# Optimization experiments

Measured on AMD Instinct MI355X. Metric: run time of the kernel, lower is better.

The kernel has to match this reference:

```python
import jax, jax.numpy as jnp
import numpy as np

B, T, OBS = 16, 4095, 128
HID, NH, FF, NL = 256, 8, 1024, 4
DH = HID // NH
ACT = 32
KEPS = 0.001   # performer kernel_epsilon (generalized attention default)
LNEPS = 1e-6   # flax LayerNorm default eps


def setup_inputs() -> dict:
    key = jax.random.key(0)
    ks = list(jax.random.split(key, 16))
    s = 0.02
    r = lambda k, shape: jax.random.normal(k, shape, jnp.float32) * s
    return {
        "hidden_state": jnp.zeros((B, 1, HID), jnp.float32),
        "ins": jax.random.normal(ks[0], (B, T, OBS), jnp.float32),
        "resets": jax.random.randint(ks[1], (B,), 0, 2).astype(bool),
        "emb_W": r(ks[2], (OBS, HID)), "emb_b": jnp.zeros((HID,), jnp.float32),
        "Wq": r(ks[3], (NL, HID, NH, DH)), "bq": jnp.zeros((NL, NH, DH), jnp.float32),
        "Wk": r(ks[4], (NL, HID, NH, DH)), "bk": jnp.zeros((NL, NH, DH), jnp.float32),
        "Wv": r(ks[5], (NL, HID, NH, DH)), "bv": jnp.zeros((NL, NH, DH), jnp.float32),
        "Wo": r(ks[6], (NL, NH, DH, HID)), "bo": jnp.zeros((NL, HID), jnp.float32),
        "ln1_s": jnp.ones((NL, HID), jnp.float32), "ln1_b": jnp.zeros((NL, HID), jnp.float32),
        "W1": r(ks[7], (NL, HID, FF)), "b1": jnp.zeros((NL, FF), jnp.float32),
        "W2": r(ks[8], (NL, FF, HID)), "b2": jnp.zeros((NL, HID), jnp.float32),
        "ln2_s": jnp.ones((NL, HID), jnp.float32), "ln2_b": jnp.zeros((NL, HID), jnp.float32),
        "qp_W": r(ks[9], (HID, ACT)), "qp_b": jnp.zeros((ACT,), jnp.float32),
    }


def layer_norm(x, scale, bias):
    m = x.mean(-1, keepdims=True)
    v = ((x - m) ** 2).mean(-1, keepdims=True)
    return (x - m) * jax.lax.rsqrt(v + LNEPS) * scale + bias


def favor_attention(q, k, v):
    # FAVOR+ generalized attention with deterministic relu features (no random
    # projection, make_fast_generalized_attention defaults), bidirectional,
    # renormalized. q,k,v: [B, L, H, Dh]; feature dim M == Dh.
    qp = jax.nn.relu(q) + KEPS
    kp = jax.nn.relu(k) + KEPS
    kv = jnp.einsum('blhm,blhd->bhmd', kp, v)            # [B,H,M,Dh]
    num = jnp.einsum('blhm,bhmd->blhd', qp, kv)           # [B,L,H,Dh]
    den = jnp.einsum('blhm,bhm->blh', qp, kp.sum(axis=1))  # [B,L,H]
    return num / den[..., None]


def encoder_block(x, Wq, bq, Wk, bk, Wv, bv, Wo, bo, ln1_s, ln1_b, W1, b1, W2, b2, ln2_s, ln2_b):
    q = jnp.einsum('bld,dhm->blhm', x, Wq) + bq
    k = jnp.einsum('bld,dhm->blhm', x, Wk) + bk
    v = jnp.einsum('bld,dhm->blhm', x, Wv) + bv
    a = favor_attention(q, k, v)
    o = jnp.einsum('blhm,hmd->bld', a, Wo) + bo
    x = o + o  # faithful to source: x = attn(x); x = x + dropout(x)
    x = layer_norm(x, ln1_s, ln1_b)
    h = jax.nn.relu(x @ W1 + b1) @ W2 + b2
    h = h + h  # same residual quirk on the FFN branch
    return layer_norm(h, ln2_s, ln2_b)


def reference(hidden_state, ins, resets, emb_W, emb_b, Wq, bq, Wk, bk, Wv, bv, Wo, bo, ln1_s, ln1_b, W1, b1, W2, b2, ln2_s, ln2_b, qp_W, qp_b):
    emb = ins @ emb_W + emb_b                         # [B, T, HID]
    hs = jnp.where(resets[:, None, None], 0.0, hidden_state)
    x = jnp.concatenate([hs, emb], axis=-2)           # [B, 1+T, HID]
    for i in range(NL):
        x = encoder_block(x, Wq[i], bq[i], Wk[i], bk[i], Wv[i], bv[i], Wo[i], bo[i],
                          ln1_s[i], ln1_b[i], W1[i], b1[i], W2[i], b2[i], ln2_s[i], ln2_b[i])
    new_hidden = x[..., 0:1, :]                       # carry token
    q_vals = new_hidden @ qp_W + qp_b                 # [B, 1, ACT]
    return new_hidden, q_vals
```

## Files before the change

### kernel.cpp

```cpp
#include <hip/hip_runtime.h>


typedef unsigned short bf16_t;
typedef __attribute__((ext_vector_type(8))) short short8;
typedef __attribute__((ext_vector_type(4))) float float4v;

#define NB 16
#define LSEQ 4096
#define MROWS (NB * LSEQ)
#define HIDD 256
#define NHEAD 8
#define DHEAD 32
#define FFD 1024
#define NLAY 4
#define KEPS_F 1e-3f
#define LNEPS_F 1e-6f
#define KV_ELEMS (NB * NHEAD * 32 * 33)

__device__ __forceinline__ float b2f(bf16_t h) {
    return __uint_as_float(((unsigned int)h) << 16);
}
__device__ __forceinline__ bf16_t f2b(float f) {
    unsigned int u = __float_as_uint(f);
    u += 0x7fffu + ((u >> 16) & 1u);
    return (bf16_t)(u >> 16);
}

#define GLOAD_LDS16(g, l)                                                     \
    __builtin_amdgcn_global_load_lds(                                         \
        (const __attribute__((address_space(1))) void*)(g),                   \
        (__attribute__((address_space(3))) void*)(l), 16, 0, 0)

__global__ __launch_bounds__(256) void conv_transpose_kernel(
    const float* __restrict__ in, bf16_t* __restrict__ out, int R, int C,
    size_t ils, size_t ols)
{
    __shared__ float tile[32][33];
    const size_t ib = (size_t)blockIdx.z * ils;
    const size_t ob = (size_t)blockIdx.z * ols;
    const int r0 = blockIdx.y * 32, c0 = blockIdx.x * 32;
    const int tx = threadIdx.x & 31, ty = threadIdx.x >> 5;
#pragma unroll
    for (int rr = ty; rr < 32; rr += 8)
        tile[rr][tx] = in[ib + (size_t)(r0 + rr) * C + c0 + tx];
    __syncthreads();
#pragma unroll
    for (int rr = ty; rr < 32; rr += 8)
        out[ob + (size_t)(c0 + rr) * R + r0 + tx] = f2b(tile[tx][rr]);
}

__global__ __launch_bounds__(256) void concat_bias_kernel(
    const float* __restrict__ bq, const float* __restrict__ bk,
    const float* __restrict__ bv, float* __restrict__ bqkv)
{
    const int l = blockIdx.x, j = threadIdx.x;
    bqkv[l * 768 + j]       = bq[l * 256 + j];
    bqkv[l * 768 + 256 + j] = bk[l * 256 + j];
    bqkv[l * 768 + 512 + j] = bv[l * 256 + j];
}

__global__ __launch_bounds__(256) void prep_a_kernel(
    const float* __restrict__ ins, bf16_t* __restrict__ Ain)
{
    const int row = blockIdx.x * 2 + (threadIdx.x >> 7);
    const int j = threadIdx.x & 127;
    const int b = row >> 12, l = row & (LSEQ - 1);
    bf16_t v = 0;
    if (l != 0) v = f2b(ins[((size_t)b * 4095 + (l - 1)) * 128 + j]);
    Ain[(size_t)row * 128 + j] = v;
}

__global__ __launch_bounds__(256) void fix_row0_kernel(
    const float* __restrict__ hidden, const int* __restrict__ resets,
    bf16_t* __restrict__ X)
{
    const int b = blockIdx.x, j = threadIdx.x;
    float v = resets[b] ? 0.f : hidden[b * HIDD + j];
    X[((size_t)b * LSEQ) * HIDD + j] = f2b(v);
}

template <int MODE>
__global__ __launch_bounds__(512) void gemm_mfma(
    const bf16_t* __restrict__ A, const bf16_t* __restrict__ WT,
    const float* __restrict__ bias, bf16_t* __restrict__ C,
    int M, int N, int K, int lda, int ldc)
{
    __shared__ __align__(16) bf16_t As[128 * 64];
    __shared__ __align__(16) bf16_t Bs[256 * 64];
    const int tid = threadIdx.x;
    const int wave = tid >> 6, lane = tid & 63;

    const int Nn = N >> 8;
    const int id = blockIdx.x;
    const int s = id >> 3;
    const int bm = ((id & 7) + ((s / Nn) << 3)) * 128;
    const int bn = (s % Nn) * 256;

    const int quad = lane >> 4, mr = lane & 15;
    const int mxor = mr & 7;
    const int wm0 = (wave & 1) * 64;
    const int wn0 = (wave >> 1) * 64;

    float4v acc[4][4];
#pragma unroll
    for (int i = 0; i < 4; i++)
#pragma unroll
        for (int j = 0; j < 4; j++) acc[i][j] = (float4v)(0.f);

    for (int k0 = 0; k0 < K; k0 += 64) {
#pragma unroll
        for (int it = 0; it < 2; it++) {
            const int c = it * 512 + tid;
            const int r = c >> 3;
            const int kofs = ((c & 7) ^ (r & 7)) * 8;
            GLOAD_LDS16(A + (size_t)(bm + r) * lda + k0 + kofs, &As[c * 8]);
        }
#pragma unroll
        for (int it = 0; it < 4; it++) {
            const int c = it * 512 + tid;
            const int r = c >> 3;
            const int kofs = ((c & 7) ^ (r & 7)) * 8;
            GLOAD_LDS16(WT + (size_t)(bn + r) * K + k0 + kofs, &Bs[c * 8]);
        }
        __syncthreads();
#pragma unroll
        for (int kk = 0; kk < 8; kk += 4) {
            short8 a[4], b[4];
#pragma unroll
            for (int i = 0; i < 4; i++)
                a[i] = *(const short8*)&As[((wm0 + i * 16 + mr) * 8 + ((quad + kk) ^ mxor)) * 8];
#pragma unroll
            for (int j = 0; j < 4; j++)
                b[j] = *(const short8*)&Bs[((wn0 + j * 16 + mr) * 8 + ((quad + kk) ^ mxor)) * 8];
#pragma unroll
            for (int i = 0; i < 4; i++)
#pragma unroll
                for (int j = 0; j < 4; j++)
                    acc[i][j] = __builtin_amdgcn_mfma_f32_16x16x32_bf16(
                        a[i], b[j], acc[i][j], 0, 0, 0);
        }
        __syncthreads();
    }

    float bcol[4];
#pragma unroll
    for (int j = 0; j < 4; j++) bcol[j] = bias[bn + wn0 + j * 16 + mr];
#pragma unroll
    for (int i = 0; i < 4; i++) {
#pragma unroll
        for (int r = 0; r < 4; r++) {
            const int grow = bm + wm0 + i * 16 + quad * 4 + r;
            bf16_t* crow = C + (size_t)grow * ldc + bn + wn0 + mr;
#pragma unroll
            for (int j = 0; j < 4; j++) {
                float v = acc[i][j][r] + bcol[j];
                if (MODE == 1) v = fmaxf(v, 0.f);
                crow[j * 16] = f2b(v);
            }
        }
    }
}

__global__ __launch_bounds__(512) void gemm_ln_mfma(
    const bf16_t* __restrict__ A, const bf16_t* __restrict__ WT,
    const float* __restrict__ bias, const float* __restrict__ sc,
    const float* __restrict__ bi, bf16_t* __restrict__ out,
    int K, int lda)
{
    __shared__ __align__(16) bf16_t As[128 * 64];
    __shared__ __align__(16) bf16_t Bs[256 * 64];
    __shared__ float red[8][64][2];
    __shared__ float fin[128][2];

    const int tid = threadIdx.x;
    const int wave = tid >> 6, lane = tid & 63;
    const int bm = blockIdx.x * 128;
    const int quad = lane >> 4, mr = lane & 15;
    const int mxor = mr & 7;
    const int wm0 = (wave & 1) * 64;
    const int wn0 = (wave >> 1) * 64;

    float4v acc[4][4];
#pragma unroll
    for (int i = 0; i < 4; i++)
#pragma unroll
        for (int j = 0; j < 4; j++) acc[i][j] = (float4v)(0.f);

    for (int k0 = 0; k0 < K; k0 += 64) {
#pragma unroll
        for (int it = 0; it < 6; it++) {
            const int c = it * 512 + tid;
            if (c < 1024) {
                const int r = c >> 3;
                const int kofs = ((c & 7) ^ (r & 7)) * 8;
                GLOAD_LDS16(A + (size_t)(bm + r) * lda + k0 + kofs, &As[c * 8]);
            } else {
                const int cb = c - 1024;
                const int r = cb >> 3;
                const int kofs = ((cb & 7) ^ (r & 7)) * 8;
                GLOAD_LDS16(WT + (size_t)r * K + k0 + kofs, &Bs[cb * 8]);
            }
        }
        __syncthreads();
#pragma unroll
        for (int kk = 0; kk < 8; kk += 4) {
            short8 a[4], b[4];
#pragma unroll
            for (int i = 0; i < 4; i++)
                a[i] = *(const short8*)&As[((wm0 + i * 16 + mr) * 8 + ((quad + kk) ^ mxor)) * 8];
#pragma unroll
            for (int j = 0; j < 4; j++)
                b[j] = *(const short8*)&Bs[((wn0 + j * 16 + mr) * 8 + ((quad + kk) ^ mxor)) * 8];
#pragma unroll
            for (int i = 0; i < 4; i++)
#pragma unroll
                for (int j = 0; j < 4; j++)
                    acc[i][j] = __builtin_amdgcn_mfma_f32_16x16x32_bf16(
                        a[i], b[j], acc[i][j], 0, 0, 0);
        }
        __syncthreads();
    }

    float bcol[4];
#pragma unroll
    for (int j = 0; j < 4; j++) bcol[j] = bias[wn0 + j * 16 + mr];

#pragma unroll
    for (int i = 0; i < 4; i++) {
#pragma unroll
        for (int r = 0; r < 4; r++) {
            float s = 0.f, s2 = 0.f;
#pragma unroll
            for (int j = 0; j < 4; j++) {
                const float v = 2.0f * (acc[i][j][r] + bcol[j]);
                s += v; s2 += v * v;
            }
#pragma unroll
            for (int off = 1; off < 16; off <<= 1) {
                s  += __shfl_xor(s, off, 64);
                s2 += __shfl_xor(s2, off, 64);
            }
            if (mr == 0) {
                const int rl = i * 16 + quad * 4 + r;
                red[wave][rl][0] = s;
                red[wave][rl][1] = s2;
            }
        }
    }
    __syncthreads();
    if (tid < 256) {
        const int R = tid >> 1, p = tid & 1;
        const int mh = R >> 6, rl = R & 63;
        fin[R][p] = red[mh][rl][p] + red[mh + 2][rl][p]
                  + red[mh + 4][rl][p] + red[mh + 6][rl][p];
    }
    __syncthreads();

    float scv[4], biv[4];
#pragma unroll
    for (int j = 0; j < 4; j++) {
        scv[j] = sc[wn0 + j * 16 + mr];
        biv[j] = bi[wn0 + j * 16 + mr];
    }
#pragma unroll
    for (int i = 0; i < 4; i++) {
#pragma unroll
        for (int r = 0; r < 4; r++) {
            const int R = wm0 + i * 16 + quad * 4 + r;
            const float mean = fin[R][0] * (1.0f / 256.0f);
            const float var  = fin[R][1] * (1.0f / 256.0f) - mean * mean;
            const float rs = rsqrtf(var + LNEPS_F);
            bf16_t* crow = out + (size_t)(bm + R) * 256 + wn0 + mr;
#pragma unroll
            for (int j = 0; j < 4; j++) {
                const float v = 2.0f * (acc[i][j][r] + bcol[j]);
                crow[j * 16] = f2b((v - mean) * rs * scv[j] + biv[j]);
            }
        }
    }
}

__global__ __launch_bounds__(512) void gemm_favor_ln_mfma(
    const bf16_t* __restrict__ QKV, const float* __restrict__ KV,
    const bf16_t* __restrict__ WT, const float* __restrict__ bias,
    const float* __restrict__ sc, const float* __restrict__ bi,
    bf16_t* __restrict__ out)
{
    __shared__ __align__(16) bf16_t As[128 * 64];
    __shared__ __align__(16) bf16_t Bs[256 * 64];
    __shared__ __align__(16) bf16_t kvT[NHEAD * 34 * 36];
    __shared__ float red[8][64][2];
    __shared__ float fin[128][2];

    const int tid = threadIdx.x;
    const int wave = tid >> 6, lane = tid & 63;
    const int bm = blockIdx.x * 128;
    const int b = bm >> 12;
    const int quad = lane >> 4, mr = lane & 15;
    const int mxor = mr & 7;
    const int wm0 = (wave & 1) * 64;
    const int wn0 = (wave >> 1) * 64;

    for (int e = tid; e < NHEAD * 34 * 32; e += 512) {
        const int h = e / (34 * 32);
        const int rem = e - h * (34 * 32);
        const int d = rem >> 5, m = rem & 31;
        bf16_t v = 0;
        if (d < 33) v = f2b(KV[((size_t)(b * NHEAD + h)) * (32 * 33) + m * 33 + d]);
        kvT[(h * 34 + d) * 36 + m] = v;
    }
    __syncthreads();

    float4v acc[4][4];
#pragma unroll
    for (int i = 0; i < 4; i++)
#pragma unroll
        for (int j = 0; j < 4; j++) acc[i][j] = (float4v)(0.f);

    for (int k0 = 0; k0 < 256; k0 += 64) {
#pragma unroll
        for (int it = 0; it < 4; it++) {
            const int c = it * 512 + tid;
            const int r = c >> 3;
            const int kofs = ((c & 7) ^ (r & 7)) * 8;
            GLOAD_LDS16(WT + (size_t)r * 256 + k0 + kofs, &Bs[c * 8]);
        }
        const int h0 = k0 >> 5;
        const int Rrow = bm + wave * 16 + mr;
#pragma unroll
        for (int hh = 0; hh < 2; hh++) {
            const int h = h0 + hh;
            short8 araw = *(const short8*)(QKV + (size_t)Rrow * 768 + h * 32 + quad * 8);
            short8 a;
#pragma unroll
            for (int j = 0; j < 8; j++)
                a[j] = (short)f2b(fmaxf(b2f((bf16_t)araw[j]), 0.f) + KEPS_F);
            short8 bf0 = *(const short8*)&kvT[(h * 34 + mr) * 36 + quad * 8];
            short8 bf1 = *(const short8*)&kvT[(h * 34 + 16 + mr) * 36 + quad * 8];
            short8 bden;
#pragma unroll
            for (int j = 0; j < 8; j++) bden[j] = 0;
            if (mr == 0)
                bden = *(const short8*)&kvT[(h * 34 + 32) * 36 + quad * 8];
            float4v c0 = __builtin_amdgcn_mfma_f32_16x16x32_bf16(a, bf0, (float4v)(0.f), 0, 0, 0);
            float4v c1 = __builtin_amdgcn_mfma_f32_16x16x32_bf16(a, bf1, (float4v)(0.f), 0, 0, 0);
            float4v c2 = __builtin_amdgcn_mfma_f32_16x16x32_bf16(a, bden, (float4v)(0.f), 0, 0, 0);
#pragma unroll
            for (int r = 0; r < 4; r++) {
                const float den = __shfl(c2[r], quad << 4);
                const float rinv = 1.0f / den;
                const int R = wave * 16 + quad * 4 + r;
                const int ca = hh * 32 + mr;
                const int cbn = hh * 32 + 16 + mr;
                As[(R * 8 + ((ca >> 3) ^ (R & 7))) * 8 + (ca & 7)]   = f2b(c0[r] * rinv);
                As[(R * 8 + ((cbn >> 3) ^ (R & 7))) * 8 + (cbn & 7)] = f2b(c1[r] * rinv);
            }
        }
        __syncthreads();
#pragma unroll
        for (int kk = 0; kk < 8; kk += 4) {
            short8 a[4], bfr[4];
#pragma unroll
            for (int i = 0; i < 4; i++)
                a[i] = *(const short8*)&As[((wm0 + i * 16 + mr) * 8 + ((quad + kk) ^ mxor)) * 8];
#pragma unroll
            for (int j = 0; j < 4; j++)
                bfr[j] = *(const short8*)&Bs[((wn0 + j * 16 + mr) * 8 + ((quad + kk) ^ mxor)) * 8];
#pragma unroll
            for (int i = 0; i < 4; i++)
#pragma unroll
                for (int j = 0; j < 4; j++)
                    acc[i][j] = __builtin_amdgcn_mfma_f32_16x16x32_bf16(
                        a[i], bfr[j], acc[i][j], 0, 0, 0);
        }
        __syncthreads();
    }

    float bcol[4];
#pragma unroll
    for (int j = 0; j < 4; j++) bcol[j] = bias[wn0 + j * 16 + mr];

#pragma unroll
    for (int i = 0; i < 4; i++) {
#pragma unroll
        for (int r = 0; r < 4; r++) {
            float s = 0.f, s2 = 0.f;
#pragma unroll
            for (int j = 0; j < 4; j++) {
                const float v = 2.0f * (acc[i][j][r] + bcol[j]);
                s += v; s2 += v * v;
            }
#pragma unroll
            for (int off = 1; off < 16; off <<= 1) {
                s  += __shfl_xor(s, off, 64);
                s2 += __shfl_xor(s2, off, 64);
            }
            if (mr == 0) {
                const int rl = i * 16 + quad * 4 + r;
                red[wave][rl][0] = s;
                red[wave][rl][1] = s2;
            }
        }
    }
    __syncthreads();
    if (tid < 256) {
        const int R = tid >> 1, p = tid & 1;
        const int mh = R >> 6, rl = R & 63;
        fin[R][p] = red[mh][rl][p] + red[mh + 2][rl][p]
                  + red[mh + 4][rl][p] + red[mh + 6][rl][p];
    }
    __syncthreads();

    float scv[4], biv[4];
#pragma unroll
    for (int j = 0; j < 4; j++) {
        scv[j] = sc[wn0 + j * 16 + mr];
        biv[j] = bi[wn0 + j * 16 + mr];
    }
#pragma unroll
    for (int i = 0; i < 4; i++) {
#pragma unroll
        for (int r = 0; r < 4; r++) {
            const int R = wm0 + i * 16 + quad * 4 + r;
            const float mean = fin[R][0] * (1.0f / 256.0f);
            const float var  = fin[R][1] * (1.0f / 256.0f) - mean * mean;
            const float rs = rsqrtf(var + LNEPS_F);
            bf16_t* crow = out + (size_t)(bm + R) * 256 + wn0 + mr;
#pragma unroll
            for (int j = 0; j < 4; j++) {
                const float v = 2.0f * (acc[i][j][r] + bcol[j]);
                crow[j * 16] = f2b((v - mean) * rs * scv[j] + biv[j]);
            }
        }
    }
}

__global__ __launch_bounds__(256) void zero_kv(float* __restrict__ KV)
{
    int i = blockIdx.x * 256 + threadIdx.x;
    if (i < KV_ELEMS) KV[i] = 0.f;
}

__global__ __launch_bounds__(256) void kv_mfma(
    const bf16_t* __restrict__ QKV, float* __restrict__ KV)
{
    __shared__ __align__(16) char smem[24576];
    bf16_t (*kp)[36] = (bf16_t(*)[36])smem;
    bf16_t (*vv)[52] = (bf16_t(*)[52])(smem + 9216);
    float (*red)[6][64][4] = (float(*)[6][64][4])smem;

    const int bh = blockIdx.x;
    const int b = bh >> 3, h = bh & 7;
    const size_t rowbase = (size_t)b * LSEQ + blockIdx.y * 512;
    const int tid = threadIdx.x;
    const int wave = tid >> 6, lane = tid & 63;
    const int quad = lane >> 4, mr = lane & 15;

    for (int e = tid; e < 128 * 20; e += 256) {
        const int l = e / 20, c = 32 + (e % 20);
        vv[l][c] = (c == 32) ? (bf16_t)0x3F80 : (bf16_t)0;
    }

    float4v acc[2][3];
#pragma unroll
    for (int i = 0; i < 2; i++)
#pragma unroll
        for (int t = 0; t < 3; t++) acc[i][t] = (float4v)(0.f);

    for (int pass = 0; pass < 4; pass++) {
        __syncthreads();
        const size_t lp = rowbase + pass * 128;
#pragma unroll
        for (int it = 0; it < 4; it++) {
            const int e = tid + it * 256;
            const int l = e >> 3, c0 = (e & 7) * 4;
            const bf16_t* src = QKV + (lp + l) * 768 + 256 + h * 32 + c0;
            ushort4 kq = *(const ushort4*)src;
            ushort4 vq = *(const ushort4*)(src + 256);
            ushort4 ko;
            ko.x = f2b(fmaxf(b2f(kq.x), 0.f) + KEPS_F);
            ko.y = f2b(fmaxf(b2f(kq.y), 0.f) + KEPS_F);
            ko.z = f2b(fmaxf(b2f(kq.z), 0.f) + KEPS_F);
            ko.w = f2b(fmaxf(b2f(kq.w), 0.f) + KEPS_F);
            *(ushort4*)&kp[l][c0] = ko;
            *(ushort4*)&vv[l][c0] = vq;
        }
        __syncthreads();

        const int lw = wave * 32 + quad * 8;
        short8 a[2], bb[3];
#pragma unroll
        for (int i = 0; i < 2; i++)
#pragma unroll
            for (int j = 0; j < 8; j++)
                a[i][j] = (short)kp[lw + j][i * 16 + mr];
#pragma unroll
        for (int t = 0; t < 3; t++)
#pragma unroll
            for (int j = 0; j < 8; j++)
                bb[t][j] = (short)vv[lw + j][t * 16 + mr];
#pragma unroll
        for (int i = 0; i < 2; i++)
#pragma unroll
            for (int t = 0; t < 3; t++)
                acc[i][t] = __builtin_amdgcn_mfma_f32_16x16x32_bf16(
                    a[i], bb[t], acc[i][t], 0, 0, 0);
    }

    __syncthreads();
#pragma unroll
    for (int i = 0; i < 2; i++)
#pragma unroll
        for (int t = 0; t < 3; t++)
#pragma unroll
            for (int r = 0; r < 4; r++)
                red[wave][i * 3 + t][lane][r] = acc[i][t][r];
    __syncthreads();

    float* dst = KV + (size_t)bh * (32 * 33);
    for (int e = tid; e < 6 * 64 * 4; e += 256) {
        const int t = e >> 8, li = (e >> 2) & 63, r = e & 3;
        const float s = red[0][t][li][r] + red[1][t][li][r]
                      + red[2][t][li][r] + red[3][t][li][r];
        const int i = t / 3, j = t % 3;
        const int m = i * 16 + (li >> 4) * 4 + r;
        const int d = j * 16 + (li & 15);
        if (d < 33) atomicAdd(&dst[m * 33 + d], s);
    }
}

__global__ __launch_bounds__(256) void head_kernel(
    const bf16_t* __restrict__ X, const float* __restrict__ qpW,
    const float* __restrict__ qpb, float* __restrict__ out)
{
    const int b = blockIdx.x, j = threadIdx.x;
    __shared__ float xr[HIDD];
    float v = b2f(X[((size_t)b * LSEQ) * HIDD + j]);
    xr[j] = v;
    out[b * HIDD + j] = v;
    __syncthreads();
    if (j < 32) {
        float acc = qpb[j];
        for (int d = 0; d < HIDD; d++)
            acc = fmaf(xr[d], qpW[d * 32 + j], acc);
        out[NB * HIDD + b * 32 + j] = acc;
    }
}

extern "C" void kernel_launch(void* const* d_in, const int* in_sizes, int n_in,
                              void* d_out, int out_size, void* d_ws, size_t ws_size,
                              hipStream_t stream)
{
    const float* hidden = (const float*)d_in[0];
    const float* ins    = (const float*)d_in[1];
    const int*   resets = (const int*)d_in[2];
    const float* embW   = (const float*)d_in[3];
    const float* embb   = (const float*)d_in[4];
    const float* Wq = (const float*)d_in[5];
    const float* bq = (const float*)d_in[6];
    const float* Wk = (const float*)d_in[7];
    const float* bk = (const float*)d_in[8];
    const float* Wv = (const float*)d_in[9];
    const float* bv = (const float*)d_in[10];
    const float* Wo = (const float*)d_in[11];
    const float* bo = (const float*)d_in[12];
    const float* ln1s = (const float*)d_in[13];
    const float* ln1b = (const float*)d_in[14];
    const float* W1 = (const float*)d_in[15];
    const float* b1 = (const float*)d_in[16];
    const float* W2 = (const float*)d_in[17];
    const float* b2 = (const float*)d_in[18];
    const float* ln2s = (const float*)d_in[19];
    const float* ln2b = (const float*)d_in[20];
    const float* qpW = (const float*)d_in[21];
    const float* qpb = (const float*)d_in[22];

    const size_t ACT_SZ = (size_t)MROWS * HIDD;
    bf16_t* X    = (bf16_t*)d_ws;
    bf16_t* QKV  = X + ACT_SZ;
    bf16_t* H1   = QKV;
    bf16_t* Ain  = QKV;
    float*  KV   = (float*)(QKV + (size_t)MROWS * FFD);
    float*  bqkv = KV + KV_ELEMS;
    bf16_t* WqkvT = (bf16_t*)(bqkv + NLAY * 768);
    bf16_t* WoT   = WqkvT + (size_t)NLAY * 3 * HIDD * HIDD;
    bf16_t* W1T   = WoT + (size_t)NLAY * HIDD * HIDD;
    bf16_t* W2T   = W1T + (size_t)NLAY * HIDD * FFD;
    bf16_t* embWT = W2T + (size_t)NLAY * FFD * HIDD;

    const dim3 blk(256);
    const dim3 blk512(512);
    const size_t HH = (size_t)HIDD * HIDD;

    conv_transpose_kernel<<<dim3(8, 8, NLAY), blk, 0, stream>>>(Wq, WqkvT,          HIDD, HIDD, HH, 3 * HH);
    conv_transpose_kernel<<<dim3(8, 8, NLAY), blk, 0, stream>>>(Wk, WqkvT + HH,     HIDD, HIDD, HH, 3 * HH);
    conv_transpose_kernel<<<dim3(8, 8, NLAY), blk, 0, stream>>>(Wv, WqkvT + 2 * HH, HIDD, HIDD, HH, 3 * HH);
    conv_transpose_kernel<<<dim3(8, 8, NLAY), blk, 0, stream>>>(Wo, WoT, HIDD, HIDD, HH, HH);
    conv_transpose_kernel<<<dim3(32, 8, NLAY), blk, 0, stream>>>(W1, W1T, HIDD, FFD, (size_t)HIDD * FFD, (size_t)HIDD * FFD);
    conv_transpose_kernel<<<dim3(8, 32, NLAY), blk, 0, stream>>>(W2, W2T, FFD, HIDD, (size_t)HIDD * FFD, (size_t)HIDD * FFD);
    conv_transpose_kernel<<<dim3(8, 4, 1), blk, 0, stream>>>(embW, embWT, 128, HIDD, 0, 0);
    concat_bias_kernel<<<NLAY, blk, 0, stream>>>(bq, bk, bv, bqkv);

    prep_a_kernel<<<MROWS / 2, blk, 0, stream>>>(ins, Ain);
    gemm_mfma<0><<<dim3(512), blk512, 0, stream>>>(Ain, embWT, embb, X, MROWS, HIDD, 128, 128, HIDD);
    fix_row0_kernel<<<NB, blk, 0, stream>>>(hidden, resets, X);

    for (int l = 0; l < NLAY; l++) {
        gemm_mfma<0><<<dim3(512 * 3), blk512, 0, stream>>>(X, WqkvT + (size_t)l * 3 * HH,
                                                           bqkv + l * 768, QKV, MROWS, 768, HIDD, HIDD, 768);

        zero_kv<<<(KV_ELEMS + 255) / 256, blk, 0, stream>>>(KV);
        kv_mfma<<<dim3(NB * NHEAD, 8), blk, 0, stream>>>(QKV, KV);

        gemm_favor_ln_mfma<<<MROWS / 128, blk512, 0, stream>>>(
            QKV, KV, WoT + (size_t)l * HH, bo + l * HIDD,
            ln1s + l * HIDD, ln1b + l * HIDD, X);

        gemm_mfma<1><<<dim3(512 * 4), blk512, 0, stream>>>(X, W1T + (size_t)l * HIDD * FFD,
                                                           b1 + l * FFD, H1, MROWS, FFD, HIDD, HIDD, FFD);
        gemm_ln_mfma<<<MROWS / 128, blk512, 0, stream>>>(
            H1, W2T + (size_t)l * FFD * HIDD, b2 + l * HIDD,
            ln2s + l * HIDD, ln2b + l * HIDD, X, FFD, FFD);
    }

    head_kernel<<<NB, blk, 0, stream>>>(X, qpW, qpb, (float*)d_out);
}
```

Before: 1.011 ms.

## Use 256x256 tiles with 4-stage async LDS pipeline in dense GEMMs

Replaces the 128x256 single-buffered GEMM and GEMM+LayerNorm kernels with 256x256 tiles, K-step 32, and a four-deep ring of LDS buffers. Global-to-LDS loads are issued three steps ahead and waited on with explicit vmcnt counts and barriers, with MFMA blocks raised in priority. The goal is to hide memory latency and halve B-tile reloads per output. In exchange it uses much more LDS and accumulator registers, which limits occupancy, and it relies on fragile hand-tuned wait counts.

Result: slower. 1.078 ms (+6.6%).

```diff
diff --git a/kernel.cpp b/kernel.cpp
--- a/kernel.cpp
+++ b/kernel.cpp
@@ -31,6 +31,17 @@
         (const __attribute__((address_space(1))) void*)(g),                   \
         (__attribute__((address_space(3))) void*)(l), 16, 0, 0)
 
+#define SBAR() __builtin_amdgcn_s_barrier()
+#define WAITV(n)                                                              \
+    do {                                                                      \
+        asm volatile("s_waitcnt vmcnt(" #n ")" ::: "memory");                 \
+        __builtin_amdgcn_sched_barrier(0);                                    \
+    } while (0)
+
+#define FRAG16(L, R)                                                          \
+    (*(const short8*)&(L)[((((R) >> 1) * 8) +                                  \
+        (((((R) & 1) << 2) | quad) ^ (((R) >> 1) & 7))) * 8])
+
 __global__ __launch_bounds__(256) void conv_transpose_kernel(
     const float* __restrict__ in, bf16_t* __restrict__ out, int R, int C,
     size_t ils, size_t ols)
@@ -80,79 +91,119 @@
 }
 
 template <int MODE>
-__global__ __launch_bounds__(512) void gemm_mfma(
+__global__ __launch_bounds__(512, 2) void gemm_mfma256(
     const bf16_t* __restrict__ A, const bf16_t* __restrict__ WT,
     const float* __restrict__ bias, bf16_t* __restrict__ C,
     int M, int N, int K, int lda, int ldc)
 {
-    __shared__ __align__(16) bf16_t As[128 * 64];
-    __shared__ __align__(16) bf16_t Bs[256 * 64];
+    __shared__ __align__(16) bf16_t As[4][256 * 32];
+    __shared__ __align__(16) bf16_t Bs[4][256 * 32];
+
     const int tid = threadIdx.x;
     const int wave = tid >> 6, lane = tid & 63;
+    const int quad = lane >> 4, mr = lane & 15;
 
     const int Nn = N >> 8;
     const int id = blockIdx.x;
     const int s = id >> 3;
-    const int bm = ((id & 7) + ((s / Nn) << 3)) * 128;
-    const int bn = (s % Nn) * 256;
-
-    const int quad = lane >> 4, mr = lane & 15;
-    const int mxor = mr & 7;
-    const int wm0 = (wave & 1) * 64;
-    const int wn0 = (wave >> 1) * 64;
-
-    float4v acc[4][4];
-#pragma unroll
-    for (int i = 0; i < 4; i++)
+    const int bm = (((id & 7) + ((s / Nn) << 3))) << 8;
+    const int bn = (s % Nn) << 8;
+
+    const int wm = (wave & 1) << 7;
+    const int wn = (wave >> 1) << 6;
+
+    const int KT = K >> 5;
+
+    float bcol[4];
+#pragma unroll
+    for (int j = 0; j < 4; ++j) bcol[j] = bias[bn + wn + j * 16 + mr];
+    asm volatile("s_waitcnt vmcnt(0)" ::: "memory");
+    __builtin_amdgcn_sched_barrier(0);
+
+    auto stageA = [&](int t) {
+        const int k0 = t << 5;
+        bf16_t* L = &As[t & 3][0];
+#pragma unroll
+        for (int it = 0; it < 2; ++it) {
+            const int c = it * 512 + tid;
+            const int r = c >> 2;
+            const int up = ((((r & 1) << 2) | (c & 3)) ^ ((r >> 1) & 7));
+            const int grow = ((r >> 1) << 1) | (up >> 2);
+            GLOAD_LDS16(A + (size_t)(bm + grow) * lda + k0 + ((up & 3) << 3),
+                        L + c * 8);
+        }
+    };
+    auto stageB = [&](int t) {
+        const int k0 = t << 5;
+        bf16_t* L = &Bs[t & 3][0];
+#pragma unroll
+        for (int it = 0; it < 2; ++it) {
+            const int c = it * 512 + tid;
+            const int r = c >> 2;
+            const int up = ((((r & 1) << 2) | (c & 3)) ^ ((r >> 1) & 7));
+            const int grow = ((r >> 1) << 1) | (up >> 2);
+            GLOAD_LDS16(WT + (size_t)(bn + grow) * K + k0 + ((up & 3) << 3),
+                        L + c * 8);
+        }
+    };
+
+    float4v acc[8][4];
+#pragma unroll
+    for (int i = 0; i < 8; i++)
 #pragma unroll
         for (int j = 0; j < 4; j++) acc[i][j] = (float4v)(0.f);
 
-    for (int k0 = 0; k0 < K; k0 += 64) {
-#pragma unroll
-        for (int it = 0; it < 2; it++) {
-            const int c = it * 512 + tid;
-            const int r = c >> 3;
-            const int kofs = ((c & 7) ^ (r & 7)) * 8;
-            GLOAD_LDS16(A + (size_t)(bm + r) * lda + k0 + kofs, &As[c * 8]);
-        }
-#pragma unroll
-        for (int it = 0; it < 4; it++) {
-            const int c = it * 512 + tid;
-            const int r = c >> 3;
-            const int kofs = ((c & 7) ^ (r & 7)) * 8;
-            GLOAD_LDS16(WT + (size_t)(bn + r) * K + k0 + kofs, &Bs[c * 8]);
-        }
-        __syncthreads();
-#pragma unroll
-        for (int kk = 0; kk < 8; kk += 4) {
-            short8 a[4], b[4];
-#pragma unroll
-            for (int i = 0; i < 4; i++)
-                a[i] = *(const short8*)&As[((wm0 + i * 16 + mr) * 8 + ((quad + kk) ^ mxor)) * 8];
-#pragma unroll
-            for (int j = 0; j < 4; j++)
-                b[j] = *(const short8*)&Bs[((wn0 + j * 16 + mr) * 8 + ((quad + kk) ^ mxor)) * 8];
-#pragma unroll
-            for (int i = 0; i < 4; i++)
-#pragma unroll
-                for (int j = 0; j < 4; j++)
-                    acc[i][j] = __builtin_amdgcn_mfma_f32_16x16x32_bf16(
-                        a[i], b[j], acc[i][j], 0, 0, 0);
-        }
-        __syncthreads();
-    }
-
-    float bcol[4];
-#pragma unroll
-    for (int j = 0; j < 4; j++) bcol[j] = bias[bn + wn0 + j * 16 + mr];
-#pragma unroll
-    for (int i = 0; i < 4; i++) {
-#pragma unroll
-        for (int r = 0; r < 4; r++) {
-            const int grow = bm + wm0 + i * 16 + quad * 4 + r;
-            bf16_t* crow = C + (size_t)grow * ldc + bn + wn0 + mr;
-#pragma unroll
-            for (int j = 0; j < 4; j++) {
+    const int P = KT < 3 ? KT : 3;
+    for (int tt = 0; tt < P; ++tt) { stageA(tt); stageB(tt); }
+
+    for (int t = 0; t < KT; ++t) {
+        const int ahead = KT - 1 - t;
+        if (ahead >= 2) { WAITV(8); } else if (ahead == 1) { WAITV(4); } else { WAITV(0); }
+        SBAR();
+        const bf16_t* LA = &As[t & 3][0];
+        const bf16_t* LB = &Bs[t & 3][0];
+        short8 a[4], b[4];
+#pragma unroll
+        for (int j = 0; j < 4; ++j) b[j] = FRAG16(LB, wn + j * 16 + mr);
+#pragma unroll
+        for (int i = 0; i < 4; ++i) a[i] = FRAG16(LA, wm + i * 16 + mr);
+        if (t + 3 < KT) stageA(t + 3);
+        SBAR();
+        __builtin_amdgcn_s_setprio(1);
+        __builtin_amdgcn_sched_barrier(0);
+#pragma unroll
+        for (int i = 0; i < 4; ++i)
+#pragma unroll
+            for (int j = 0; j < 4; ++j)
+                acc[i][j] = __builtin_amdgcn_mfma_f32_16x16x32_bf16(
+                    a[i], b[j], acc[i][j], 0, 0, 0);
+        __builtin_amdgcn_sched_barrier(0);
+        __builtin_amdgcn_s_setprio(0);
+        SBAR();
+#pragma unroll
+        for (int i = 0; i < 4; ++i) a[i] = FRAG16(LA, wm + 64 + i * 16 + mr);
+        if (t + 3 < KT) stageB(t + 3);
+        SBAR();
+        __builtin_amdgcn_s_setprio(1);
+        __builtin_amdgcn_sched_barrier(0);
+#pragma unroll
+        for (int i = 0; i < 4; ++i)
+#pragma unroll
+            for (int j = 0; j < 4; ++j)
+                acc[4 + i][j] = __builtin_amdgcn_mfma_f32_16x16x32_bf16(
+                    a[i], b[j], acc[4 + i][j], 0, 0, 0);
+        __builtin_amdgcn_sched_barrier(0);
+        __builtin_amdgcn_s_setprio(0);
+    }
+
+#pragma unroll
+    for (int i = 0; i < 8; ++i) {
+#pragma unroll
+        for (int r = 0; r < 4; ++r) {
+            const int grow = bm + wm + i * 16 + quad * 4 + r;
+            bf16_t* crow = C + (size_t)grow * ldc + bn + wn + mr;
+#pragma unroll
+            for (int j = 0; j < 4; ++j) {
                 float v = acc[i][j][r] + bcol[j];
                 if (MODE == 1) v = fmaxf(v, 0.f);
                 crow[j * 16] = f2b(v);
@@ -161,118 +212,155 @@
     }
 }
 
-__global__ __launch_bounds__(512) void gemm_ln_mfma(
+__global__ __launch_bounds__(512, 2) void gemm_ln256(
     const bf16_t* __restrict__ A, const bf16_t* __restrict__ WT,
     const float* __restrict__ bias, const float* __restrict__ sc,
     const float* __restrict__ bi, bf16_t* __restrict__ out,
     int K, int lda)
 {
-    __shared__ __align__(16) bf16_t As[128 * 64];
-    __shared__ __align__(16) bf16_t Bs[256 * 64];
-    __shared__ float red[8][64][2];
-    __shared__ float fin[128][2];
+    __shared__ __align__(16) bf16_t As[4][256 * 32];
+    __shared__ __align__(16) bf16_t Bs[4][256 * 32];
+    __shared__ float red[8][128][2];
+    __shared__ float fin[256][2];
 
     const int tid = threadIdx.x;
     const int wave = tid >> 6, lane = tid & 63;
-    const int bm = blockIdx.x * 128;
     const int quad = lane >> 4, mr = lane & 15;
-    const int mxor = mr & 7;
-    const int wm0 = (wave & 1) * 64;
-    const int wn0 = (wave >> 1) * 64;
-
-    float4v acc[4][4];
-#pragma unroll
-    for (int i = 0; i < 4; i++)
+    const int bm = blockIdx.x << 8;
+
+    const int wm = (wave & 1) << 7;
+    const int wn = (wave >> 1) << 6;
+
+    const int KT = K >> 5;
+
+    float bcol[4], scv[4], biv[4];
+#pragma unroll
+    for (int j = 0; j < 4; ++j) {
+        bcol[j] = bias[wn + j * 16 + mr];
+        scv[j]  = sc[wn + j * 16 + mr];
+        biv[j]  = bi[wn + j * 16 + mr];
+    }
+    asm volatile("s_waitcnt vmcnt(0)" ::: "memory");
+    __builtin_amdgcn_sched_barrier(0);
+
+    auto stageA = [&](int t) {
+        const int k0 = t << 5;
+        bf16_t* L = &As[t & 3][0];
+#pragma unroll
+        for (int it = 0; it < 2; ++it) {
+            const int c = it * 512 + tid;
+            const int r = c >> 2;
+            const int up = ((((r & 1) << 2) | (c & 3)) ^ ((r >> 1) & 7));
+            const int grow = ((r >> 1) << 1) | (up >> 2);
+            GLOAD_LDS16(A + (size_t)(bm + grow) * lda + k0 + ((up & 3) << 3),
+                        L + c * 8);
+        }
+    };
+    auto stageB = [&](int t) {
+        const int k0 = t << 5;
+        bf16_t* L = &Bs[t & 3][0];
+#pragma unroll
+        for (int it = 0; it < 2; ++it) {
+            const int c = it * 512 + tid;
+            const int r = c >> 2;
+            const int up = ((((r & 1) << 2) | (c & 3)) ^ ((r >> 1) & 7));
+            const int grow = ((r >> 1) << 1) | (up >> 2);
+            GLOAD_LDS16(WT + (size_t)grow * K + k0 + ((up & 3) << 3),
+                        L + c * 8);
+        }
+    };
+
+    float4v acc[8][4];
+#pragma unroll
+    for (int i = 0; i < 8; i++)
 #pragma unroll
         for (int j = 0; j < 4; j++) acc[i][j] = (float4v)(0.f);
 
-    for (int k0 = 0; k0 < K; k0 += 64) {
-#pragma unroll
-        for (int it = 0; it < 6; it++) {
-            const int c = it * 512 + tid;
-            if (c < 1024) {
-                const int r = c >> 3;
-                const int kofs = ((c & 7) ^ (r & 7)) * 8;
-                GLOAD_LDS16(A + (size_t)(bm + r) * lda + k0 + kofs, &As[c * 8]);
-            } else {
-                const int cb = c - 1024;
-                const int r = cb >> 3;
-                const int kofs = ((cb & 7) ^ (r & 7)) * 8;
-                GLOAD_LDS16(WT + (size_t)r * K + k0 + kofs, &Bs[cb * 8]);
-            }
-        }
-        __syncthreads();
-#pragma unroll
-        for (int kk = 0; kk < 8; kk += 4) {
-            short8 a[4], b[4];
-#pragma unroll
-            for (int i = 0; i < 4; i++)
-                a[i] = *(const short8*)&As[((wm0 + i * 16 + mr) * 8 + ((quad + kk) ^ mxor)) * 8];
-#pragma unroll
-            for (int j = 0; j < 4; j++)
-                b[j] = *(const short8*)&Bs[((wn0 + j * 16 + mr) * 8 + ((quad + kk) ^ mxor)) * 8];
-#pragma unroll
-            for (int i = 0; i < 4; i++)
-#pragma unroll
-                for (int j = 0; j < 4; j++)
-                    acc[i][j] = __builtin_amdgcn_mfma_f32_16x16x32_bf16(
-                        a[i], b[j], acc[i][j], 0, 0, 0);
-        }
-        __syncthreads();
-    }
-
-    float bcol[4];
-#pragma unroll
-    for (int j = 0; j < 4; j++) bcol[j] = bias[wn0 + j * 16 + mr];
-
-#pragma unroll
-    for (int i = 0; i < 4; i++) {
-#pragma unroll
-        for (int r = 0; r < 4; r++) {
-            float s = 0.f, s2 = 0.f;
-#pragma unroll
-            for (int j = 0; j < 4; j++) {
+    const int P = KT < 3 ? KT : 3;
+    for (int tt = 0; tt < P; ++tt) { stageA(tt); stageB(tt); }
+
+    for (int t = 0; t < KT; ++t) {
+        const int ahead = KT - 1 - t;
+        if (ahead >= 2) { WAITV(8); } else if (ahead == 1) { WAITV(4); } else { WAITV(0); }
+        SBAR();
+        const bf16_t* LA = &As[t & 3][0];
+        const bf16_t* LB = &Bs[t & 3][0];
+        short8 a[4], b[4];
+#pragma unroll
+        for (int j = 0; j < 4; ++j) b[j] = FRAG16(LB, wn + j * 16 + mr);
+#pragma unroll
+        for (int i = 0; i < 4; ++i) a[i] = FRAG16(LA, wm + i * 16 + mr);
+        if (t + 3 < KT) stageA(t + 3);
+        SBAR();
+        __builtin_amdgcn_s_setprio(1);
+        __builtin_amdgcn_sched_barrier(0);
+#pragma unroll
+        for (int i = 0; i < 4; ++i)
+#pragma unroll
+            for (int j = 0; j < 4; ++j)
+                acc[i][j] = __builtin_amdgcn_mfma_f32_16x16x32_bf16(
+                    a[i], b[j], acc[i][j], 0, 0, 0);
+        __builtin_amdgcn_sched_barrier(0);
+        __builtin_amdgcn_s_setprio(0);
+        SBAR();
+#pragma unroll
+        for (int i = 0; i < 4; ++i) a[i] = FRAG16(LA, wm + 64 + i * 16 + mr);
+        if (t + 3 < KT) stageB(t + 3);
+        SBAR();
+        __builtin_amdgcn_s_setprio(1);
+        __builtin_amdgcn_sched_barrier(0);
+#pragma unroll
+        for (int i = 0; i < 4; ++i)
+#pragma unroll
+            for (int j = 0; j < 4; ++j)
+                acc[4 + i][j] = __builtin_amdgcn_mfma_f32_16x16x32_bf16(
+                    a[i], b[j], acc[4 + i][j], 0, 0, 0);
+        __builtin_amdgcn_sched_barrier(0);
+        __builtin_amdgcn_s_setprio(0);
+    }
+
+#pragma unroll
+    for (int i = 0; i < 8; ++i) {
+#pragma unroll
+        for (int r = 0; r < 4; ++r) {
+            float ss = 0.f, s2 = 0.f;
+#pragma unroll
+            for (int j = 0; j < 4; ++j) {
                 const float v = 2.0f * (acc[i][j][r] + bcol[j]);
-                s += v; s2 += v * v;
+                ss += v; s2 += v * v;
             }
 #pragma unroll
             for (int off = 1; off < 16; off <<= 1) {
-                s  += __shfl_xor(s, off, 64);
+                ss += __shfl_xor(ss, off, 64);
                 s2 += __shfl_xor(s2, off, 64);
             }
             if (mr == 0) {
                 const int rl = i * 16 + quad * 4 + r;
-                red[wave][rl][0] = s;
+                red[wave][rl][0] = ss;
                 red[wave][rl][1] = s2;
             }
         }
     }
     __syncthreads();
-    if (tid < 256) {
+    {
         const int R = tid >> 1, p = tid & 1;
-        const int mh = R >> 6, rl = R & 63;
+        const int mh = R >> 7, rl = R & 127;
         fin[R][p] = red[mh][rl][p] + red[mh + 2][rl][p]
                   + red[mh + 4][rl][p] + red[mh + 6][rl][p];
     }
     __syncthreads();
 
-    float scv[4], biv[4];
-#pragma unroll
-    for (int j = 0; j < 4; j++) {
-        scv[j] = sc[wn0 + j * 16 + mr];
-        biv[j] = bi[wn0 + j * 16 + mr];
-    }
-#pragma unroll
-    for (int i = 0; i < 4; i++) {
-#pragma unroll
-        for (int r = 0; r < 4; r++) {
-            const int R = wm0 + i * 16 + quad * 4 + r;
+#pragma unroll
+    for (int i = 0; i < 8; ++i) {
+#pragma unroll
+        for (int r = 0; r < 4; ++r) {
+            const int R = wm + i * 16 + quad * 4 + r;
             const float mean = fin[R][0] * (1.0f / 256.0f);
             const float var  = fin[R][1] * (1.0f / 256.0f) - mean * mean;
             const float rs = rsqrtf(var + LNEPS_F);
-            bf16_t* crow = out + (size_t)(bm + R) * 256 + wn0 + mr;
-#pragma unroll
-            for (int j = 0; j < 4; j++) {
+            bf16_t* crow = out + (size_t)(bm + R) * 256 + wn + mr;
+#pragma unroll
+            for (int j = 0; j < 4; ++j) {
                 const float v = 2.0f * (acc[i][j][r] + bcol[j]);
                 crow[j * 16] = f2b((v - mean) * rs * scv[j] + biv[j]);
             }
@@ -602,12 +690,12 @@
     concat_bias_kernel<<<NLAY, blk, 0, stream>>>(bq, bk, bv, bqkv);
 
     prep_a_kernel<<<MROWS / 2, blk, 0, stream>>>(ins, Ain);
-    gemm_mfma<0><<<dim3(512), blk512, 0, stream>>>(Ain, embWT, embb, X, MROWS, HIDD, 128, 128, HIDD);
+    gemm_mfma256<0><<<dim3(256), blk512, 0, stream>>>(Ain, embWT, embb, X, MROWS, HIDD, 128, 128, HIDD);
     fix_row0_kernel<<<NB, blk, 0, stream>>>(hidden, resets, X);
 
     for (int l = 0; l < NLAY; l++) {
-        gemm_mfma<0><<<dim3(512 * 3), blk512, 0, stream>>>(X, WqkvT + (size_t)l * 3 * HH,
-                                                           bqkv + l * 768, QKV, MROWS, 768, HIDD, HIDD, 768);
+        gemm_mfma256<0><<<dim3(256 * 3), blk512, 0, stream>>>(X, WqkvT + (size_t)l * 3 * HH,
+                                                              bqkv + l * 768, QKV, MROWS, 768, HIDD, HIDD, 768);
 
         zero_kv<<<(KV_ELEMS + 255) / 256, blk, 0, stream>>>(KV);
         kv_mfma<<<dim3(NB * NHEAD, 8), blk, 0, stream>>>(QKV, KV);
@@ -616,9 +704,9 @@
             QKV, KV, WoT + (size_t)l * HH, bo + l * HIDD,
             ln1s + l * HIDD, ln1b + l * HIDD, X);
 
-        gemm_mfma<1><<<dim3(512 * 4), blk512, 0, stream>>>(X, W1T + (size_t)l * HIDD * FFD,
-                                                           b1 + l * FFD, H1, MROWS, FFD, HIDD, HIDD, FFD);
-        gemm_ln_mfma<<<MROWS / 128, blk512, 0, stream>>>(
+        gemm_mfma256<1><<<dim3(256 * 4), blk512, 0, stream>>>(X, W1T + (size_t)l * HIDD * FFD,
+                                                              b1 + l * FFD, H1, MROWS, FFD, HIDD, HIDD, FFD);
+        gemm_ln256<<<dim3(256), blk512, 0, stream>>>(
             H1, W2T + (size_t)l * FFD * HIDD, b2 + l * HIDD,
             ln2s + l * HIDD, ln2b + l * HIDD, X, FFD, FFD);
     }
```
